# Optimization experiments

Hardware: AMD Instinct MI355X
Metric: run time of the kernel (lower is better)

The kernel has to match this reference:

```python
import jax, jax.numpy as jnp
from jax import lax
import numpy as np

N, T, C, H, W, S = 1, 8, 64, 192, 192, 4
HS, WS = H // S, W // S
CH = C * S * S          # 1024 = channels
G = 4                   # n_groups
CG = CH // G            # 256 = n_group_channels
ORF = 2.0               # offset_range_factor


def _unfold(x, s=S):
    # F.unfold(kernel=s, stride=s): (n,c,h,w) -> (n, c*s*s, (h//s)*(w//s))
    n, c, h, w = x.shape
    x = x.reshape(n, c, h // s, s, w // s, s).transpose(0, 1, 3, 5, 2, 4)
    return x.reshape(n, c * s * s, (h // s) * (w // s))


def _fold(x, h, w, s=S):
    # inverse of _unfold (non-overlapping)
    n, cl, _ = x.shape
    c = cl // (s * s)
    x = x.reshape(n, c, s, s, h // s, w // s).transpose(0, 1, 4, 2, 5, 3)
    return x.reshape(n, c, h, w)


def _gather_hw(x, iy, ix):
    # x (B,C,H,W); iy/ix (B,Hg,Wg) int32 -> (B,C,Hg,Wg)
    B, Cc, Hh, Ww = x.shape
    idx = (iy * Ww + ix).reshape(B, 1, -1)
    v = jnp.take_along_axis(x.reshape(B, Cc, Hh * Ww), idx, axis=2)
    return v.reshape(B, Cc, iy.shape[1], iy.shape[2])


def gs_nearest(x, grid):
    # F.grid_sample(mode='nearest', padding='zeros', align_corners=True)
    B, Cc, Hh, Ww = x.shape
    ix = (grid[..., 0] + 1.0) * 0.5 * (Ww - 1)
    iy = (grid[..., 1] + 1.0) * 0.5 * (Hh - 1)
    ixn = jnp.round(ix).astype(jnp.int32)
    iyn = jnp.round(iy).astype(jnp.int32)
    valid = (ixn >= 0) & (ixn < Ww) & (iyn >= 0) & (iyn < Hh)
    v = _gather_hw(x, jnp.clip(iyn, 0, Hh - 1), jnp.clip(ixn, 0, Ww - 1))
    return v * valid[:, None].astype(x.dtype)


def gs_bilinear(x, grid):
    # F.grid_sample(mode='bilinear', padding='zeros', align_corners=True)
    B, Cc, Hh, Ww = x.shape
    ix = (grid[..., 0] + 1.0) * 0.5 * (Ww - 1)
    iy = (grid[..., 1] + 1.0) * 0.5 * (Hh - 1)
    x0 = jnp.floor(ix)
    y0 = jnp.floor(iy)
    wx = ix - x0
    wy = iy - y0
    x0 = x0.astype(jnp.int32)
    y0 = y0.astype(jnp.int32)
    out = jnp.zeros((B, Cc) + grid.shape[1:3], x.dtype)
    for dy, dx in ((0, 0), (0, 1), (1, 0), (1, 1)):
        yi = y0 + dy
        xi = x0 + dx
        wgt = (wy if dy else 1.0 - wy) * (wx if dx else 1.0 - wx)
        valid = (xi >= 0) & (xi < Ww) & (yi >= 0) & (yi < Hh)
        v = _gather_hw(x, jnp.clip(yi, 0, Hh - 1), jnp.clip(xi, 0, Ww - 1))
        out = out + v * (wgt * valid)[:, None].astype(x.dtype)
    return out


def conv(x, w, b=None, pad=0, groups=1):
    y = lax.conv_general_dilated(x, w, (1, 1), [(pad, pad), (pad, pad)],
                                 dimension_numbers=('NCHW', 'OIHW', 'NCHW'),
                                 feature_group_count=groups)
    return y if b is None else y + b[None, :, None, None]


def ln_c(x, g, b, eps=1e-5):
    # LayerNormProxy: LayerNorm over channel dim of NCHW
    m = x.mean(axis=1, keepdims=True)
    v = ((x - m) ** 2).mean(axis=1, keepdims=True)
    return (x - m) / jnp.sqrt(v + eps) * g[None, :, None, None] + b[None, :, None, None]


def l2n(x, axis):
    return x / jnp.maximum(jnp.linalg.norm(x, axis=axis, keepdims=True), 1e-12)


def refpts(B, Hk, Wk, dt):
    ry = (jnp.linspace(0.5, Hk - 0.5, Hk, dtype=dt) / Hk) * 2 - 1
    rx = (jnp.linspace(0.5, Wk - 0.5, Wk, dtype=dt) / Wk) * 2 - 1
    ref = jnp.stack(jnp.meshgrid(ry, rx, indexing='ij'), axis=-1)  # (Hk,Wk,2)=(y,x)
    return jnp.broadcast_to(ref[None], (B, Hk, Wk, 2))


def _forward(cf, idx1, af, s1, s2, s3, loc, wtdw, btdw, lng, lnb, wtpw, wfus, bfus):
    n, c, h, w = af.shape
    t = s1.shape[1]
    hs, ws = h // S, w // S
    fl = c * S * S           # feat_len = 1024
    fn = hs * ws             # feat_num
    # trajectory locations -> normalized nearest-sampling grid
    gf = loc.reshape(n, t, 2, hs, ws).transpose(0, 1, 3, 4, 2)
    gx = 2.0 * gf[..., 0] / max(ws - 1, 1) - 1.0
    gy = 2.0 * gf[..., 1] / max(hs - 1, 1) - 1.0
    grid = jnp.stack((gx, gy), axis=-1).reshape(n * t, hs, ws, 2)
    o1 = gs_nearest(s1.reshape(n * t, fl, hs, ws), grid)
    o2 = gs_nearest(s2.reshape(n * t, fl, hs, ws), grid)
    o3 = gs_nearest(s3.reshape(n * t, fl, hs, ws), grid)
    oi = gs_nearest(idx1.reshape(n * t, fl, hs, ws), grid)
    oi = l2n(oi.reshape(n, t, fl, fn).transpose(0, 3, 1, 2), 3)   # (n,fn,t,fl)
    cu = _unfold(cf)                                              # (n,fl,fn)
    cn = l2n(cu.transpose(0, 2, 1), 2)                            # (n,fn,fl)
    tq = cn.reshape(n, hs, ws, fl).transpose(0, 3, 1, 2)          # (n,fl,hs,ws)
    tk = oi.transpose(0, 2, 1, 3).reshape(n * t, hs, ws, fl).transpose(0, 3, 1, 2)
    # deformable time offsets (grouped)
    qo = jnp.tile(tq.reshape(n * G, CG, hs, ws), (t, 1, 1, 1))
    ko = tk.reshape(n * t * G, CG, hs, ws)
    off = jnp.concatenate([qo, ko], axis=1)
    o = conv(off, wtdw, btdw, pad=2, groups=CG)
    o = ln_c(o, lng, lnb)
    o = jax.nn.gelu(o, approximate=False)
    o = conv(o, wtpw)                                             # (b,2,Hk,Wk)
    Hk, Wk = o.shape[2], o.shape[3]
    o = jnp.tanh(o) * jnp.array([1.0 / Hk, 1.0 / Wk], o.dtype).reshape(1, 2, 1, 1) * ORF
    pos = o.transpose(0, 2, 3, 1) + refpts(n * t * G, Hk, Wk, o.dtype)  # (b,Hk,Wk,(y,x))
    gp = pos[..., ::-1]                                           # (x,y) for grid_sample
    ks_ = gs_bilinear(tk.reshape(n * t * G, CG, hs, ws), gp)
    # '(n t g) c h w -> n (h w) t (g c)'
    ks_ = ks_.reshape(n, t, G, CG, Hk, Wk).transpose(0, 4, 5, 1, 2, 3).reshape(n, fn, t, fl)
    mat = jnp.einsum('nftc,nfc->nft', ks_, cn)
    csoft = mat.max(axis=2)
    cidx = mat.argmax(axis=2)
    csoft_f = _fold(jnp.broadcast_to(csoft[:, None, :], (n, fl, fn)), h, w)

    def sg(os_):
        v = gs_bilinear(os_.reshape(n * t * G, CG, hs, ws), gp).reshape(n, t, fl, fn)
        v = jnp.take_along_axis(v, cidx[:, None, None, :], axis=1)[:, 0]
        return _fold(v, h, w)

    out = conv(jnp.concatenate([sg(o1), sg(o2), sg(o3)], axis=1), wfus, bfus, pad=1)
    return out * csoft_f + af


def setup_inputs() -> dict:
    key = jax.random.key(0)
    ks = jax.random.split(key, 12)
    sc = 0.05
    return {
        'curr_feat': jax.random.normal(ks[0], (N, C, H, W), jnp.float32),
        'index_feat_set_s1': jax.random.normal(ks[1], (N, T, CH, HS, WS), jnp.float32),
        'anchor_feat': jax.random.normal(ks[2], (N, C, H, W), jnp.float32),
        'sparse_feat_set_s1': jax.random.normal(ks[3], (N, T, CH, HS, WS), jnp.float32),
        'sparse_feat_set_s2': jax.random.normal(ks[4], (N, T, CH, HS, WS), jnp.float32),
        'sparse_feat_set_s3': jax.random.normal(ks[5], (N, T, CH, HS, WS), jnp.float32),
        'location_feat': jax.random.uniform(ks[6], (N, 2 * T, HS, WS), jnp.float32) * (WS - 1.0),
        'w_tdw': jax.random.normal(ks[7], (CG, 2, 5, 5), jnp.float32) * sc,
        'b_tdw': jnp.zeros((CG,), jnp.float32),
        'ln_g': jnp.ones((CG,), jnp.float32),
        'ln_b': jnp.zeros((CG,), jnp.float32),
        'w_tpw': jax.random.normal(ks[8], (2, CG, 1, 1), jnp.float32) * sc,
        'w_fus': jax.random.normal(ks[9], (C, 3 * C, 3, 3), jnp.float32) * sc,
        'b_fus': jnp.zeros((C,), jnp.float32),
    }


def reference(curr_feat, index_feat_set_s1, anchor_feat, sparse_feat_set_s1, sparse_feat_set_s2, sparse_feat_set_s3, location_feat, w_tdw, b_tdw, ln_g, ln_b, w_tpw, w_fus, b_fus):
    return _forward(curr_feat, index_feat_set_s1, anchor_feat, sparse_feat_set_s1,
                    sparse_feat_set_s2, sparse_feat_set_s3, location_feat,
                    w_tdw, b_tdw, ln_g, ln_b, w_tpw, w_fus, b_fus)
```

## Files before the change

### kernel.cpp

```cpp
#include <hip/hip_runtime.h>
#include <math.h>

#define TT 8
#define FN 2304
#define FL 1024
#define HS 48

typedef __attribute__((ext_vector_type(8))) short short8;
typedef __attribute__((ext_vector_type(4))) float floatx4;

static constexpr size_t OFF_IDX1T  = 0;
static constexpr size_t OFF_SEL    = 75497472;
static constexpr size_t OFF_FIN    = 103809024;
static constexpr size_t OFF_WB     = 132713472;
static constexpr size_t OFF_NORM2  = 135497472;
static constexpr size_t OFF_PSRC   = 135571200;
static constexpr size_t OFF_PSCALE = 135644928;
static constexpr size_t OFF_CN     = 150994944;
static constexpr size_t OFF_QH     = 160432128;
static constexpr size_t OFF_SRCMAP = 165150720;
static constexpr size_t OFF_BSRC   = 165224448;
static constexpr size_t OFF_BW     = 166404096;
static constexpr size_t OFF_CSOFT  = 167583744;
static constexpr size_t OFF_CIDX   = 167592960;
static constexpr size_t OFF_CSRC   = 167602176;
static constexpr size_t OFF_CW     = 167749632;

__device__ inline ushort f2bf(float x) {
  union { float f; unsigned int u; } v; v.f = x;
  unsigned int r = (v.u + 0x7FFFu + ((v.u >> 16) & 1u)) >> 16;
  return (ushort)r;
}

__global__ void k_nearmap(const float* __restrict__ loc, int* __restrict__ srcmap,
                          float* __restrict__ norm2) {
  int idx = blockIdx.x * 256 + threadIdx.x;
  if (idx >= TT * FN) return;
  norm2[idx] = 0.f;
  int t = idx / FN, f = idx % FN;
  float lx = loc[(size_t)(t * 2 + 0) * FN + f];
  float ly = loc[(size_t)(t * 2 + 1) * FN + f];
  float gx = 2.0f * lx / 47.0f - 1.0f;
  float gy = 2.0f * ly / 47.0f - 1.0f;
  float ix = (gx + 1.0f) * 0.5f * 47.0f;
  float iy = (gy + 1.0f) * 0.5f * 47.0f;
  int ixn = __float2int_rn(ix);
  int iyn = __float2int_rn(iy);
  bool valid = (ixn >= 0) && (ixn < 48) && (iyn >= 0) && (iyn < 48);
  srcmap[idx] = valid ? (iyn * 48 + ixn) : -1;
}

__global__ __launch_bounds__(256) void k_transpose(const float* __restrict__ in, float* __restrict__ out,
                                                   float* __restrict__ norm2) {
  __shared__ float tile[64][65];
  const int t = blockIdx.z;
  const int cl0 = blockIdx.x * 64;
  const int f0 = blockIdx.y * 64;
  const float* src = in + (size_t)t * FL * FN;
  float* dst = out + (size_t)t * FN * FL;
  const int tx = threadIdx.x & 15, ty = threadIdx.x >> 4;
#pragma unroll
  for (int k = 0; k < 4; k++) {
    const float4 v = *reinterpret_cast<const float4*>(src + (size_t)(cl0 + ty + 16 * k) * FN + f0 + tx * 4);
    float* tr = &tile[ty + 16 * k][tx * 4];
    tr[0] = v.x; tr[1] = v.y; tr[2] = v.z; tr[3] = v.w;
  }
  __syncthreads();
#pragma unroll
  for (int k = 0; k < 4; k++) {
    float4 v;
    v.x = tile[tx * 4 + 0][ty + 16 * k];
    v.y = tile[tx * 4 + 1][ty + 16 * k];
    v.z = tile[tx * 4 + 2][ty + 16 * k];
    v.w = tile[tx * 4 + 3][ty + 16 * k];
    *reinterpret_cast<float4*>(dst + (size_t)(f0 + ty + 16 * k) * FL + cl0 + tx * 4) = v;
    float ss = v.x * v.x + v.y * v.y + v.z * v.z + v.w * v.w;
    ss += __shfl_xor(ss, 1, 64);
    ss += __shfl_xor(ss, 2, 64);
    ss += __shfl_xor(ss, 4, 64);
    ss += __shfl_xor(ss, 8, 64);
    if (tx == 0) atomicAdd(&norm2[(size_t)t * FN + f0 + ty + 16 * k], ss);
  }
}

__global__ void k_pos(const int* __restrict__ srcmap, const float* __restrict__ norm2,
                      int* __restrict__ psrc, float* __restrict__ pscale) {
  int idx = blockIdx.x * 256 + threadIdx.x;
  if (idx >= TT * FN) return;
  int s = srcmap[idx];
  int t = idx / FN;
  if (s < 0) {
    psrc[idx] = 0; pscale[idx] = 0.f;
  } else {
    psrc[idx] = s;
    float n2 = norm2[t * FN + s];
    pscale[idx] = 1.0f / fmaxf(sqrtf(n2), 1e-12f);
  }
}

__global__ __launch_bounds__(256) void k_cn(const float* __restrict__ cf, float* __restrict__ cn) {
  __shared__ float red[4];
  int f = blockIdx.x;
  int i = f / 48, j = f % 48;
  int tid = threadIdx.x;
  float v[4];
  float sq = 0.f;
#pragma unroll
  for (int k = 0; k < 4; k++) {
    int cl = tid + 256 * k;
    int c = cl >> 4, sy = (cl >> 2) & 3, sx = cl & 3;
    v[k] = cf[(size_t)c * 36864 + (size_t)(i * 4 + sy) * 192 + (j * 4 + sx)];
    sq += v[k] * v[k];
  }
#pragma unroll
  for (int m = 1; m <= 32; m <<= 1) sq += __shfl_xor(sq, m, 64);
  int lane = tid & 63, w = tid >> 6;
  if (lane == 0) red[w] = sq;
  __syncthreads();
  float total = red[0] + red[1] + red[2] + red[3];
  float scale = 1.0f / fmaxf(sqrtf(total), 1e-12f);
#pragma unroll
  for (int k = 0; k < 4; k++) cn[(size_t)f * FL + tid + 256 * k] = v[k] * scale;
}

__global__ __launch_bounds__(128) void k_qconv(const float* __restrict__ cn,
                                               const float* __restrict__ wtdw,
                                               const float* __restrict__ btdw,
                                               float* __restrict__ qhalf) {
  const int i = blockIdx.x;
  const int xcd = i & 7;
  const int sl = i >> 3;
  const int g = xcd >> 1;
  const int r0 = (xcd & 1) * 72 + sl;
  const int y = r0 / 3;
  const int xt = r0 - y * 3;
  const int j = threadIdx.x;
  const int x0 = xt * 16;
  float w0[25], w1[25];
  {
    const float* wp = wtdw + (size_t)j * 50;
#pragma unroll
    for (int p = 0; p < 25; ++p) { w0[p] = wp[p]; w1[p] = wp[25 + p]; }
  }
  float acc[16];
#pragma unroll
  for (int i2 = 0; i2 < 16; ++i2) acc[i2] = 0.f;
  const int cbase = g * 256 + 2 * j;
#pragma unroll
  for (int r = 0; r < 5; ++r) {
    const int yy = y - 2 + r;
    if (yy < 0 || yy >= 48) continue;
#pragma unroll
    for (int cc2 = 0; cc2 < 20; ++cc2) {
      const int xx = x0 - 2 + cc2;
      float vx = 0.f, vy = 0.f;
      if (xx >= 0 && xx < 48) {
        const float2 v = *reinterpret_cast<const float2*>(cn + ((size_t)(yy * 48 + xx) << 10) + cbase);
        vx = v.x; vy = v.y;
      }
#pragma unroll
      for (int kx = 0; kx < 5; ++kx) {
        const int xo = cc2 - kx;
        if (xo >= 0 && xo < 16)
          acc[xo] = fmaf(vx, w0[r * 5 + kx], fmaf(vy, w1[r * 5 + kx], acc[xo]));
      }
    }
  }
  const float bb = btdw[j];
#pragma unroll
  for (int xo = 0; xo < 16; ++xo)
    qhalf[((size_t)g * FN + (y * 48 + x0 + xo)) * 128 + j] = acc[xo] + bb;
}

__global__ __launch_bounds__(128) void k_kconv_ln(const float* __restrict__ idx1t,
                                                  const int* __restrict__ psrc,
                                                  const float* __restrict__ pscale,
                                                  const float* __restrict__ wtdw,
                                                  const float* __restrict__ btdw,
                                                  const float* __restrict__ qhalf,
                                                  const float* __restrict__ lng,
                                                  const float* __restrict__ lnb,
                                                  const float* __restrict__ wtpw,
                                                  int* __restrict__ bsrc,
                                                  float* __restrict__ bw) {
  __shared__ float ch[16][257];
  __shared__ int   s_ps[100];
  __shared__ float s_sc[100];
  const int ib = blockIdx.x;
  const int xcd = ib & 7;
  const int sl = ib >> 3;
  const int b = xcd + 8 * (sl / 144);
  const int r0 = sl % 144;
  const int y = r0 / 3;
  const int xt = r0 - y * 3;
  const int t = b >> 2, g = b & 3;
  const int j = threadIdx.x;
  const int x0 = xt * 16;
  const int tp = t * FN;

  if (j < 100) {
    const int rr = j / 20, cc = j - rr * 20;
    const int yy = y - 2 + rr, xx = x0 - 2 + cc;
    int sv = 0; float sc = 0.f;
    if ((unsigned)yy < 48u && (unsigned)xx < 48u) {
      const int p = tp + yy * 48 + xx;
      sv = psrc[p]; sc = pscale[p];
    }
    s_ps[j] = sv; s_sc[j] = sc;
  }

  float w0[25], w1[25];
  {
    const float* wp = wtdw + (size_t)(128 + j) * 50;
#pragma unroll
    for (int p = 0; p < 25; ++p) { w0[p] = wp[p]; w1[p] = wp[25 + p]; }
  }
  float acc[16];
#pragma unroll
  for (int i2 = 0; i2 < 16; ++i2) acc[i2] = 0.f;
  const int cbase = g * 256 + 2 * j;
  __syncthreads();
#pragma unroll
  for (int r = 0; r < 5; ++r) {
    const int yy = y - 2 + r;
    if (yy < 0 || yy >= 48) continue;
#pragma unroll
    for (int cc2 = 0; cc2 < 20; ++cc2) {
      const int s2 = s_ps[r * 20 + cc2];
      const float sc = s_sc[r * 20 + cc2];
      const float2 v = *reinterpret_cast<const float2*>(idx1t + (((size_t)tp + s2) << 10) + cbase);
      const float vx = v.x * sc, vy = v.y * sc;
#pragma unroll
      for (int kx = 0; kx < 5; ++kx) {
        const int xo = cc2 - kx;
        if (xo >= 0 && xo < 16)
          acc[xo] = fmaf(vx, w0[r * 5 + kx], fmaf(vy, w1[r * 5 + kx], acc[xo]));
      }
    }
  }
  const float bb = btdw[128 + j];
#pragma unroll
  for (int xo = 0; xo < 16; ++xo) ch[xo][128 + j] = acc[xo] + bb;
#pragma unroll
  for (int xo = 0; xo < 16; ++xo)
    ch[xo][j] = qhalf[((size_t)g * FN + (y * 48 + x0 + xo)) * 128 + j];
  __syncthreads();

  const int lane = j & 63, wv = j >> 6;
  for (int p = wv; p < 16; p += 2) {
    float v0 = ch[p][lane], v1 = ch[p][lane + 64], v2 = ch[p][lane + 128], v3 = ch[p][lane + 192];
    float s = v0 + v1 + v2 + v3;
    float q = v0 * v0 + v1 * v1 + v2 * v2 + v3 * v3;
#pragma unroll
    for (int m = 1; m <= 32; m <<= 1) { s += __shfl_xor(s, m, 64); q += __shfl_xor(q, m, 64); }
    float mean = s * (1.0f / 256.0f);
    float var = q * (1.0f / 256.0f) - mean * mean;
    float rstd = rsqrtf(var + 1e-5f);
    float d0 = 0.f, d1 = 0.f;
#pragma unroll
    for (int k2 = 0; k2 < 4; k2++) {
      int c = lane + 64 * k2;
      float xv = (k2 == 0) ? v0 : (k2 == 1) ? v1 : (k2 == 2) ? v2 : v3;
      float xn = (xv - mean) * rstd * lng[c] + lnb[c];
      float ge = 0.5f * xn * (1.0f + erff(xn * 0.70710678118654752440f));
      d0 += ge * wtpw[c];
      d1 += ge * wtpw[256 + c];
    }
#pragma unroll
    for (int m = 1; m <= 32; m <<= 1) { d0 += __shfl_xor(d0, m, 64); d1 += __shfl_xor(d1, m, 64); }
    if (lane == 0) {
      float o0 = tanhf(d0) * (2.0f / 48.0f);
      float o1 = tanhf(d1) * (2.0f / 48.0f);
      int x = x0 + p;
      float ry = (0.5f + (float)y) / 48.0f * 2.0f - 1.0f;
      float rx = (0.5f + (float)x) / 48.0f * 2.0f - 1.0f;
      float pos0 = o0 + ry, pos1 = o1 + rx;
      float ix = (pos1 + 1.0f) * 0.5f * 47.0f;
      float iy = (pos0 + 1.0f) * 0.5f * 47.0f;
      float x0f = floorf(ix), y0f = floorf(iy);
      float wx = ix - x0f, wy = iy - y0f;
      int xi = (int)x0f, yi = (int)y0f;
      size_t base = ((size_t)b * FN + y * 48 + x) * 4;
#pragma unroll
      for (int c = 0; c < 4; c++) {
        int dy = c >> 1, dx = c & 1;
        int yy2 = yi + dy, xx2 = xi + dx;
        bool ok = ((unsigned)yy2 < 48u) && ((unsigned)xx2 < 48u);
        float wgt = (dy ? wy : 1.0f - wy) * (dx ? wx : 1.0f - wx);
        bsrc[base + c] = ok ? (yy2 * 48 + xx2) : -1;
        bw[base + c] = wgt;
      }
    }
  }
}

__global__ __launch_bounds__(256) void k_mat(const float* __restrict__ idx1t,
                                             const int* __restrict__ psrc,
                                             const float* __restrict__ pscale,
                                             const float* __restrict__ cn,
                                             const int* __restrict__ bsrc,
                                             const float* __restrict__ bw,
                                             float* __restrict__ csoft,
                                             int* __restrict__ cidx) {
  __shared__ float red[8][4];
  const int f = blockIdx.x;
  const int tid = threadIdx.x;
  const int lane = tid & 63, w = tid >> 6;
  const int coff = w * 256 + lane * 4;
  const float4 cnv = *reinterpret_cast<const float4*>(cn + (size_t)f * FL + coff);
#pragma unroll
  for (int t = 0; t < TT; t++) {
    const size_t mb = ((size_t)(t * 4 + w) * FN + f) * 4;
    const int4 cs = *reinterpret_cast<const int4*>(bsrc + mb);
    const float4 wv = *reinterpret_cast<const float4*>(bw + mb);
    const int tp = t * FN;
    const float* base = idx1t + ((size_t)tp << 10) + coff;
    float ax = 0.f, ay = 0.f, az = 0.f, aw = 0.f;
    if (cs.x >= 0) { const float wsc = wv.x * pscale[tp + cs.x];
      const float4 u = *reinterpret_cast<const float4*>(base + ((size_t)psrc[tp + cs.x] << 10));
      ax = fmaf(wsc, u.x, ax); ay = fmaf(wsc, u.y, ay); az = fmaf(wsc, u.z, az); aw = fmaf(wsc, u.w, aw); }
    if (cs.y >= 0) { const float wsc = wv.y * pscale[tp + cs.y];
      const float4 u = *reinterpret_cast<const float4*>(base + ((size_t)psrc[tp + cs.y] << 10));
      ax = fmaf(wsc, u.x, ax); ay = fmaf(wsc, u.y, ay); az = fmaf(wsc, u.z, az); aw = fmaf(wsc, u.w, aw); }
    if (cs.z >= 0) { const float wsc = wv.z * pscale[tp + cs.z];
      const float4 u = *reinterpret_cast<const float4*>(base + ((size_t)psrc[tp + cs.z] << 10));
      ax = fmaf(wsc, u.x, ax); ay = fmaf(wsc, u.y, ay); az = fmaf(wsc, u.z, az); aw = fmaf(wsc, u.w, aw); }
    if (cs.w >= 0) { const float wsc = wv.w * pscale[tp + cs.w];
      const float4 u = *reinterpret_cast<const float4*>(base + ((size_t)psrc[tp + cs.w] << 10));
      ax = fmaf(wsc, u.x, ax); ay = fmaf(wsc, u.y, ay); az = fmaf(wsc, u.z, az); aw = fmaf(wsc, u.w, aw); }
    float partial = ax * cnv.x + ay * cnv.y + az * cnv.z + aw * cnv.w;
#pragma unroll
    for (int m = 1; m <= 32; m <<= 1) partial += __shfl_xor(partial, m, 64);
    if (lane == 0) red[t][w] = partial;
  }
  __syncthreads();
  if (tid == 0) {
    float bestv = -INFINITY;
    int besti = 0;
#pragma unroll
    for (int t = 0; t < TT; t++) {
      float tot = red[t][0] + red[t][1] + red[t][2] + red[t][3];
      if (tot > bestv) { bestv = tot; besti = t; }
    }
    csoft[f] = bestv; cidx[f] = besti;
  }
}

__global__ void k_comp(const int* __restrict__ bsrc, const float* __restrict__ bw,
                       const int* __restrict__ cidx, const int* __restrict__ srcmap,
                       int* __restrict__ csrc, float* __restrict__ cw) {
  int idx = blockIdx.x * 256 + threadIdx.x;
  if (idx >= FN * 4) return;
  int f = idx >> 2, g = idx & 3;
  int t = cidx[f];
  int b = t * 4 + g;
  size_t mb = ((size_t)b * FN + f) * 4;
  size_t ob = (size_t)idx * 4;
#pragma unroll
  for (int c = 0; c < 4; c++) {
    int s = bsrc[mb + c];
    csrc[ob + c] = (s >= 0) ? srcmap[t * FN + s] : -1;
    cw[ob + c] = bw[mb + c];
  }
}

__global__ __launch_bounds__(256) void k_sel(const float* __restrict__ s1,
                                             const float* __restrict__ s2,
                                             const float* __restrict__ s3,
                                             const int* __restrict__ cidx,
                                             const int* __restrict__ csrc,
                                             const float* __restrict__ cw,
                                             float* __restrict__ sel) {
  __shared__ float pl[4 * FN];
  const int cl = blockIdx.x, m = blockIdx.y;
  const float* sm = (m == 0) ? s1 : (m == 1) ? s2 : s3;
  const int g = cl >> 8;
  const int tid = threadIdx.x;
  float acc[9];
  int tsel[9];
  int4 cs[9];
  float4 wv[9];
#pragma unroll
  for (int it = 0; it < 9; it++) {
    int f = tid + 256 * it;
    tsel[it] = cidx[f];
    cs[it] = *reinterpret_cast<const int4*>(csrc + ((size_t)f * 4 + g) * 4);
    wv[it] = *reinterpret_cast<const float4*>(cw + ((size_t)f * 4 + g) * 4);
    acc[it] = 0.f;
  }
  float4* pl4 = reinterpret_cast<float4*>(pl);
  for (int half = 0; half < 2; half++) {
    __syncthreads();
#pragma unroll
    for (int j = 0; j < 9; j++) {
      const int e = j * 256 + tid;
      const int tl = e / 576;
      const int r = e - tl * 576;
      const float4* src4 = reinterpret_cast<const float4*>(sm + ((size_t)(half * 4 + tl) * FL + cl) * FN);
      pl4[e] = src4[r];
    }
    __syncthreads();
#pragma unroll
    for (int it = 0; it < 9; it++) {
      const int t = tsel[it] - half * 4;
      if (t >= 0 && t < 4) {
        float a = 0.f;
        if (cs[it].x >= 0) a += wv[it].x * pl[t * FN + cs[it].x];
        if (cs[it].y >= 0) a += wv[it].y * pl[t * FN + cs[it].y];
        if (cs[it].z >= 0) a += wv[it].z * pl[t * FN + cs[it].z];
        if (cs[it].w >= 0) a += wv[it].w * pl[t * FN + cs[it].w];
        acc[it] = a;
      }
    }
  }
  __syncthreads();
#pragma unroll
  for (int it = 0; it < 9; it++) pl[tid + 256 * it] = acc[it];
  __syncthreads();
  float4* orow = reinterpret_cast<float4*>(sel + ((size_t)m * FL + cl) * FN);
#pragma unroll
  for (int e = tid; e < 576; e += 256) orow[e] = pl4[e];
}

__global__ void k_zb(unsigned int* __restrict__ fin_u) {
  int idx = blockIdx.x * 256 + threadIdx.x;
  if (idx >= 772 * 96) return;
  int bp = idx / 96, u = idx % 96;
  int yy, xx;
  if (bp < 194)      { yy = 0;   xx = bp; }
  else if (bp < 388) { yy = 193; xx = bp - 194; }
  else if (bp < 580) { yy = bp - 388 + 1; xx = 0; }
  else               { yy = bp - 580 + 1; xx = 193; }
  fin_u[((size_t)yy * 194 + xx) * 96 + u] = 0;
}

__global__ __launch_bounds__(256) void k_fold2(const float* __restrict__ sel,
                                               ushort* __restrict__ fin) {
  __shared__ float ld[256 * 49];
  const int fy = blockIdx.x;
  const int m = blockIdx.y >> 2, c2t = blockIdx.y & 3;
  const int t = threadIdx.x;
  const float* sp = sel + ((size_t)m * 1024 + c2t * 256) * 2304 + fy * 48;
#pragma unroll
  for (int j = 0; j < 12; j++) {
    const int e = t + 256 * j;
    const int cl_l = e / 12, c4 = e % 12;
    const float4 v = *reinterpret_cast<const float4*>(sp + (size_t)cl_l * 2304 + c4 * 4);
    float* dr = &ld[cl_l * 49 + c4 * 4];
    dr[0] = v.x; dr[1] = v.y; dr[2] = v.z; dr[3] = v.w;
  }
  __syncthreads();
  const int ci0 = m * 64 + c2t * 16 + (t & 3) * 4;
  const int xb = t >> 2;
#pragma unroll
  for (int py = 0; py < 4; py++) {
    for (int jx = 0; jx < 3; jx++) {
      const int x = xb + 64 * jx;
      const int px = x & 3, fx = x >> 2;
      ushort4 v;
      ushort* vp = (ushort*)&v;
#pragma unroll
      for (int jj = 0; jj < 4; jj++) {
        int cl_l = ((t & 3) * 4 + jj) * 16 + py * 4 + px;
        vp[jj] = f2bf(ld[cl_l * 49 + fx]);
      }
      *reinterpret_cast<ushort4*>(fin + (((size_t)(fy * 4 + py + 1) * 194) + x + 1) * 192 + ci0) = v;
    }
  }
}

__global__ void k_wb(const float* __restrict__ wfus, ushort* __restrict__ wb) {
  int idx = blockIdx.x * 256 + threadIdx.x;
  if (idx >= 64 * 9 * 96) return;
  int cp = idx % 96, tap = (idx / 96) % 9, co = idx / (96 * 9);
  int ci = cp * 2;
  float a = wfus[((size_t)co * 192 + ci) * 9 + tap];
  float b = wfus[((size_t)co * 192 + ci + 1) * 9 + tap];
  unsigned int pk = (unsigned int)f2bf(a) | ((unsigned int)f2bf(b) << 16);
  reinterpret_cast<unsigned int*>(wb)[((size_t)co * 9 + tap) * 96 + cp] = pk;
}

__global__ __launch_bounds__(256) void k_fus(const ushort* __restrict__ fin,
                                             const ushort* __restrict__ wb,
                                             const float* __restrict__ bfus,
                                             const float* __restrict__ csoft,
                                             const float* __restrict__ af,
                                             float* __restrict__ out) {
  const int y = blockIdx.x;
  const int wv = threadIdx.x >> 6;
  const int l = threadIdx.x & 63;
  const int ln = l & 15, qd = l >> 4;
  const int x0 = wv * 48;
  floatx4 acc[4][3];
#pragma unroll
  for (int a = 0; a < 4; a++)
#pragma unroll
    for (int b = 0; b < 3; b++) acc[a][b] = (floatx4){0.f, 0.f, 0.f, 0.f};

  const int koff = qd * 8;
  for (int tap = 0; tap < 9; tap++) {
    const int ky = tap / 3, kx = tap % 3;
    const ushort* brow = fin + ((size_t)(y + ky) * 194 + kx) * 192;
    const ushort* wrow = wb + (size_t)tap * 192;
#pragma unroll
    for (int c6 = 0; c6 < 6; c6++) {
      const int ci = c6 * 32 + koff;
      short8 A[4], B[3];
#pragma unroll
      for (int mt = 0; mt < 4; mt++)
        A[mt] = *reinterpret_cast<const short8*>(wrow + (size_t)(mt * 16 + ln) * 1728 + ci);
#pragma unroll
      for (int nt = 0; nt < 3; nt++)
        B[nt] = *reinterpret_cast<const short8*>(brow + (size_t)(x0 + nt * 16 + ln) * 192 + ci);
#pragma unroll
      for (int mt = 0; mt < 4; mt++)
#pragma unroll
        for (int nt = 0; nt < 3; nt++)
          acc[mt][nt] = __builtin_amdgcn_mfma_f32_16x16x32_bf16(A[mt], B[nt], acc[mt][nt], 0, 0, 0);
    }
  }
#pragma unroll
  for (int nt = 0; nt < 3; nt++) {
    const int x = x0 + nt * 16 + ln;
    const float cs = csoft[(y >> 2) * 48 + (x >> 2)];
#pragma unroll
    for (int mt = 0; mt < 4; mt++) {
#pragma unroll
      for (int r = 0; r < 4; r++) {
        const int co = mt * 16 + qd * 4 + r;
        const size_t oi = (size_t)co * 36864 + (size_t)y * 192 + x;
        out[oi] = (acc[mt][nt][r] + bfus[co]) * cs + af[oi];
      }
    }
  }
}

extern "C" void kernel_launch(void* const* d_in, const int* in_sizes, int n_in,
                              void* d_out, int out_size, void* d_ws, size_t ws_size,
                              hipStream_t stream) {
  const float* cf   = (const float*)d_in[0];
  const float* idx1 = (const float*)d_in[1];
  const float* af   = (const float*)d_in[2];
  const float* s1   = (const float*)d_in[3];
  const float* s2   = (const float*)d_in[4];
  const float* s3   = (const float*)d_in[5];
  const float* loc  = (const float*)d_in[6];
  const float* wtdw = (const float*)d_in[7];
  const float* btdw = (const float*)d_in[8];
  const float* lng  = (const float*)d_in[9];
  const float* lnb  = (const float*)d_in[10];
  const float* wtpw = (const float*)d_in[11];
  const float* wfus = (const float*)d_in[12];
  const float* bfus = (const float*)d_in[13];
  float* out = (float*)d_out;
  char* ws = (char*)d_ws;

  float* idx1t  = (float*)(ws + OFF_IDX1T);
  float* sel    = (float*)(ws + OFF_SEL);
  ushort* fin   = (ushort*)(ws + OFF_FIN);
  ushort* wb    = (ushort*)(ws + OFF_WB);
  float* norm2  = (float*)(ws + OFF_NORM2);
  int*   psrc   = (int*)(ws + OFF_PSRC);
  float* pscale = (float*)(ws + OFF_PSCALE);
  float* cn     = (float*)(ws + OFF_CN);
  float* qh     = (float*)(ws + OFF_QH);
  int*   srcmap = (int*)(ws + OFF_SRCMAP);
  int*   bsrc   = (int*)(ws + OFF_BSRC);
  float* bw     = (float*)(ws + OFF_BW);
  float* csoft  = (float*)(ws + OFF_CSOFT);
  int*   cidx   = (int*)(ws + OFF_CIDX);
  int*   csrc   = (int*)(ws + OFF_CSRC);
  float* cw     = (float*)(ws + OFF_CW);

  k_nearmap<<<72, 256, 0, stream>>>(loc, srcmap, norm2);
  k_transpose<<<dim3(16, 36, 8), 256, 0, stream>>>(idx1, idx1t, norm2);
  k_cn<<<2304, 256, 0, stream>>>(cf, cn);
  k_pos<<<72, 256, 0, stream>>>(srcmap, norm2, psrc, pscale);
  k_wb<<<216, 256, 0, stream>>>(wfus, wb);
  k_zb<<<290, 256, 0, stream>>>((unsigned int*)fin);
  k_qconv<<<576, 128, 0, stream>>>(cn, wtdw, btdw, qh);
  k_kconv_ln<<<4608, 128, 0, stream>>>(idx1t, psrc, pscale, wtdw, btdw, qh, lng, lnb, wtpw, bsrc, bw);
  k_mat<<<2304, 256, 0, stream>>>(idx1t, psrc, pscale, cn, bsrc, bw, csoft, cidx);
  k_comp<<<36, 256, 0, stream>>>(bsrc, bw, cidx, srcmap, csrc, cw);
  k_sel<<<dim3(1024, 3), 256, 0, stream>>>(s1, s2, s3, cidx, csrc, cw, sel);
  k_fold2<<<dim3(48, 12), 256, 0, stream>>>(sel, fin);
  k_fus<<<192, 256, 0, stream>>>(fin, wb, bfus, csoft, af, out);
}
```

Measured before the change: 525.0 us.

## Double-buffer k_sel plane loads via direct global-to-LDS with packed registers

Rewrites the k_sel gather so each of the 8 time planes is streamed into a double-buffered 2xFN shared array using global_load_lds. The load of plane s+1 overlaps with computing plane s. Per-thread source indices and time selectors are bit-packed into 32-bit words and the bilinear weights are stored as half2, cutting register use. Launch bounds now target 6 blocks per CU, which together with the smaller LDS footprint is meant to raise occupancy. The trade-off is lower precision on the weights (fp16) and more barriers, one per plane instead of per half.

```diff
diff --git a/kernel.cpp b/kernel.cpp
--- a/kernel.cpp
+++ b/kernel.cpp
@@ -1,4 +1,5 @@
 #include <hip/hip_runtime.h>
+#include <hip/hip_fp16.h>
 #include <math.h>
 
 #define TT 8
@@ -30,6 +31,12 @@
   union { float f; unsigned int u; } v; v.f = x;
   unsigned int r = (v.u + 0x7FFFu + ((v.u >> 16) & 1u)) >> 16;
   return (ushort)r;
+}
+
+__device__ __forceinline__ void gload_lds16(const float* g, float* l) {
+  __builtin_amdgcn_global_load_lds(
+      (const __attribute__((address_space(1))) unsigned int*)(g),
+      (__attribute__((address_space(3))) unsigned int*)(l), 16, 0, 0);
 }
 
 __global__ void k_nearmap(const float* __restrict__ loc, int* __restrict__ srcmap,
@@ -364,61 +371,79 @@
   }
 }
 
-__global__ __launch_bounds__(256) void k_sel(const float* __restrict__ s1,
-                                             const float* __restrict__ s2,
-                                             const float* __restrict__ s3,
-                                             const int* __restrict__ cidx,
-                                             const int* __restrict__ csrc,
-                                             const float* __restrict__ cw,
-                                             float* __restrict__ sel) {
-  __shared__ float pl[4 * FN];
+__global__ __launch_bounds__(256, 6) void k_sel(const float* __restrict__ s1,
+                                                const float* __restrict__ s2,
+                                                const float* __restrict__ s3,
+                                                const int* __restrict__ cidx,
+                                                const int* __restrict__ csrc,
+                                                const float* __restrict__ cw,
+                                                float* __restrict__ sel) {
+  __shared__ float buf[2][FN];
   const int cl = blockIdx.x, m = blockIdx.y;
   const float* sm = (m == 0) ? s1 : (m == 1) ? s2 : s3;
   const int g = cl >> 8;
   const int tid = threadIdx.x;
+  const int lane = tid & 63, wid = tid >> 6;
+
+  unsigned int pk0[9], pk1[9], wh01[9], wh23[9];
   float acc[9];
-  int tsel[9];
-  int4 cs[9];
-  float4 wv[9];
 #pragma unroll
   for (int it = 0; it < 9; it++) {
-    int f = tid + 256 * it;
-    tsel[it] = cidx[f];
-    cs[it] = *reinterpret_cast<const int4*>(csrc + ((size_t)f * 4 + g) * 4);
-    wv[it] = *reinterpret_cast<const float4*>(cw + ((size_t)f * 4 + g) * 4);
+    const int f = tid + 256 * it;
+    const unsigned int ts = (unsigned int)cidx[f];
+    const int4 cs = *reinterpret_cast<const int4*>(csrc + ((size_t)f * 4 + g) * 4);
+    const float4 wv = *reinterpret_cast<const float4*>(cw + ((size_t)f * 4 + g) * 4);
+    const unsigned int c0 = (cs.x >= 0) ? (unsigned int)cs.x : 0x1FFFu;
+    const unsigned int c1 = (cs.y >= 0) ? (unsigned int)cs.y : 0x1FFFu;
+    const unsigned int c2 = (cs.z >= 0) ? (unsigned int)cs.z : 0x1FFFu;
+    const unsigned int c3 = (cs.w >= 0) ? (unsigned int)cs.w : 0x1FFFu;
+    pk0[it] = c0 | (c1 << 13) | (ts << 26);
+    pk1[it] = c2 | (c3 << 13);
+    __half2 h01 = __floats2half2_rn(wv.x, wv.y);
+    __half2 h23 = __floats2half2_rn(wv.z, wv.w);
+    wh01[it] = *reinterpret_cast<unsigned int*>(&h01);
+    wh23[it] = *reinterpret_cast<unsigned int*>(&h23);
     acc[it] = 0.f;
   }
-  float4* pl4 = reinterpret_cast<float4*>(pl);
-  for (int half = 0; half < 2; half++) {
-    __syncthreads();
-#pragma unroll
-    for (int j = 0; j < 9; j++) {
-      const int e = j * 256 + tid;
-      const int tl = e / 576;
-      const int r = e - tl * 576;
-      const float4* src4 = reinterpret_cast<const float4*>(sm + ((size_t)(half * 4 + tl) * FL + cl) * FN);
-      pl4[e] = src4[r];
-    }
-    __syncthreads();
+
+  {
+    const float* pb = sm + (size_t)cl * FN;
+    for (int c = wid; c < 9; c += 4)
+      gload_lds16(pb + c * 256 + lane * 4, &buf[0][c * 256]);
+  }
+  __syncthreads();
+
+  for (int s = 0; s < TT; s++) {
+    if (s + 1 < TT) {
+      const float* pb = sm + ((size_t)(s + 1) * FL + cl) * FN;
+      float* lb = &buf[(s + 1) & 1][0];
+      for (int c = wid; c < 9; c += 4)
+        gload_lds16(pb + c * 256 + lane * 4, lb + c * 256);
+    }
+    const float* lb = &buf[s & 1][0];
 #pragma unroll
     for (int it = 0; it < 9; it++) {
-      const int t = tsel[it] - half * 4;
-      if (t >= 0 && t < 4) {
+      if ((int)(pk0[it] >> 26) == s) {
+        const unsigned int a0 = pk0[it] & 0x1FFFu, a1 = (pk0[it] >> 13) & 0x1FFFu;
+        const unsigned int a2 = pk1[it] & 0x1FFFu, a3 = (pk1[it] >> 13) & 0x1FFFu;
+        const float2 w01 = __half22float2(*reinterpret_cast<const __half2*>(&wh01[it]));
+        const float2 w23 = __half22float2(*reinterpret_cast<const __half2*>(&wh23[it]));
         float a = 0.f;
-        if (cs[it].x >= 0) a += wv[it].x * pl[t * FN + cs[it].x];
-        if (cs[it].y >= 0) a += wv[it].y * pl[t * FN + cs[it].y];
-        if (cs[it].z >= 0) a += wv[it].z * pl[t * FN + cs[it].z];
-        if (cs[it].w >= 0) a += wv[it].w * pl[t * FN + cs[it].w];
+        if (a0 < FN) a = fmaf(w01.x, lb[a0], a);
+        if (a1 < FN) a = fmaf(w01.y, lb[a1], a);
+        if (a2 < FN) a = fmaf(w23.x, lb[a2], a);
+        if (a3 < FN) a = fmaf(w23.y, lb[a3], a);
         acc[it] = a;
       }
     }
-  }
-  __syncthreads();
-#pragma unroll
-  for (int it = 0; it < 9; it++) pl[tid + 256 * it] = acc[it];
-  __syncthreads();
+    __syncthreads();
+  }
+
+#pragma unroll
+  for (int it = 0; it < 9; it++) buf[0][tid + 256 * it] = acc[it];
+  __syncthreads();
+  const float4* pl4 = reinterpret_cast<const float4*>(&buf[0][0]);
   float4* orow = reinterpret_cast<float4*>(sel + ((size_t)m * FL + cl) * FN);
-#pragma unroll
   for (int e = tid; e < 576; e += 256) orow[e] = pl4[e];
 }
 
```

After: 683.6 us. 1.3x slower.

## Bucket positions by selected frame so k_sel loads only needed time planes

Applied to the files above, without the earlier changes.

A new single-block kernel buckets the spatial positions by their selected time index, producing a compact position list and offsets per frame. k_sel now launches one block per (frame, channel, source) and returns early for frames nobody selected. Each block loads just that frame's plane into LDS via global_load_lds DMA instead of streaming all eight planes. The block ordering is remapped across XCDs. This is meant to cut redundant global reads of unused frames. The cost is many more, smaller blocks, scattered output writes, and an extra launch. Bucket buffers reuse the bsrc workspace region after k_comp has consumed it.

```diff
diff --git a/kernel.cpp b/kernel.cpp
--- a/kernel.cpp
+++ b/kernel.cpp
@@ -1,4 +1,5 @@
 #include <hip/hip_runtime.h>
+#include <hip/hip_fp16.h>
 #include <math.h>
 
 #define TT 8
@@ -20,6 +21,8 @@
 static constexpr size_t OFF_QH     = 160432128;
 static constexpr size_t OFF_SRCMAP = 165150720;
 static constexpr size_t OFF_BSRC   = 165224448;
+static constexpr size_t OFF_FLIST  = OFF_BSRC;
+static constexpr size_t OFF_FOFF   = OFF_BSRC + 9216;
 static constexpr size_t OFF_BW     = 166404096;
 static constexpr size_t OFF_CSOFT  = 167583744;
 static constexpr size_t OFF_CIDX   = 167592960;
@@ -30,6 +33,12 @@
   union { float f; unsigned int u; } v; v.f = x;
   unsigned int r = (v.u + 0x7FFFu + ((v.u >> 16) & 1u)) >> 16;
   return (ushort)r;
+}
+
+__device__ __forceinline__ void gload_lds16(const float* g, float* l) {
+  __builtin_amdgcn_global_load_lds(
+      (const __attribute__((address_space(1))) unsigned int*)(g),
+      (__attribute__((address_space(3))) unsigned int*)(l), 16, 0, 0);
 }
 
 __global__ void k_nearmap(const float* __restrict__ loc, int* __restrict__ srcmap,
@@ -364,62 +373,69 @@
   }
 }
 
+__global__ void k_bucket(const int* __restrict__ cidx, int* __restrict__ flist,
+                         int* __restrict__ foff) {
+  __shared__ int cnt[8];
+  __shared__ int base[8];
+  const int tid = threadIdx.x;
+  if (tid < 8) cnt[tid] = 0;
+  __syncthreads();
+  for (int f = tid; f < FN; f += 256) atomicAdd(&cnt[cidx[f]], 1);
+  __syncthreads();
+  if (tid == 0) {
+    int s = 0;
+    for (int t = 0; t < 8; t++) { base[t] = s; foff[t] = s; s += cnt[t]; }
+    foff[8] = s;
+  }
+  __syncthreads();
+  for (int f = tid; f < FN; f += 256) {
+    int t = cidx[f];
+    int p = atomicAdd(&base[t], 1);
+    flist[p] = f;
+  }
+}
+
 __global__ __launch_bounds__(256) void k_sel(const float* __restrict__ s1,
                                              const float* __restrict__ s2,
                                              const float* __restrict__ s3,
-                                             const int* __restrict__ cidx,
+                                             const int* __restrict__ flist,
+                                             const int* __restrict__ foff,
                                              const int* __restrict__ csrc,
                                              const float* __restrict__ cw,
                                              float* __restrict__ sel) {
-  __shared__ float pl[4 * FN];
-  const int cl = blockIdx.x, m = blockIdx.y;
+  __shared__ float pl[FN];
+  const int i = blockIdx.x;
+  const int xcd = i & 7;
+  const int b = i >> 3;
+  const int t = b & 7;
+  const int job = xcd * 384 + (b >> 3);
+  const int m = job >> 10;
+  const int cl = job & 1023;
+  const int tid = threadIdx.x;
+  const int lane = tid & 63, wid = tid >> 6;
+
+  const int o0 = foff[t], o1 = foff[t + 1];
+  if (o0 == o1) return;
+
   const float* sm = (m == 0) ? s1 : (m == 1) ? s2 : s3;
+  const float* pb = sm + ((size_t)t * FL + cl) * FN;
+  for (int c = wid; c < 9; c += 4)
+    gload_lds16(pb + c * 256 + lane * 4, &pl[c * 256]);
+  __syncthreads();
+
   const int g = cl >> 8;
-  const int tid = threadIdx.x;
-  float acc[9];
-  int tsel[9];
-  int4 cs[9];
-  float4 wv[9];
-#pragma unroll
-  for (int it = 0; it < 9; it++) {
-    int f = tid + 256 * it;
-    tsel[it] = cidx[f];
-    cs[it] = *reinterpret_cast<const int4*>(csrc + ((size_t)f * 4 + g) * 4);
-    wv[it] = *reinterpret_cast<const float4*>(cw + ((size_t)f * 4 + g) * 4);
-    acc[it] = 0.f;
-  }
-  float4* pl4 = reinterpret_cast<float4*>(pl);
-  for (int half = 0; half < 2; half++) {
-    __syncthreads();
-#pragma unroll
-    for (int j = 0; j < 9; j++) {
-      const int e = j * 256 + tid;
-      const int tl = e / 576;
-      const int r = e - tl * 576;
-      const float4* src4 = reinterpret_cast<const float4*>(sm + ((size_t)(half * 4 + tl) * FL + cl) * FN);
-      pl4[e] = src4[r];
-    }
-    __syncthreads();
-#pragma unroll
-    for (int it = 0; it < 9; it++) {
-      const int t = tsel[it] - half * 4;
-      if (t >= 0 && t < 4) {
-        float a = 0.f;
-        if (cs[it].x >= 0) a += wv[it].x * pl[t * FN + cs[it].x];
-        if (cs[it].y >= 0) a += wv[it].y * pl[t * FN + cs[it].y];
-        if (cs[it].z >= 0) a += wv[it].z * pl[t * FN + cs[it].z];
-        if (cs[it].w >= 0) a += wv[it].w * pl[t * FN + cs[it].w];
-        acc[it] = a;
-      }
-    }
-  }
-  __syncthreads();
-#pragma unroll
-  for (int it = 0; it < 9; it++) pl[tid + 256 * it] = acc[it];
-  __syncthreads();
-  float4* orow = reinterpret_cast<float4*>(sel + ((size_t)m * FL + cl) * FN);
-#pragma unroll
-  for (int e = tid; e < 576; e += 256) orow[e] = pl4[e];
+  float* orow = sel + ((size_t)m * FL + cl) * FN;
+  for (int ii = o0 + tid; ii < o1; ii += 256) {
+    const int f = flist[ii];
+    const int4 cs = *reinterpret_cast<const int4*>(csrc + ((size_t)f * 4 + g) * 4);
+    const float4 wv = *reinterpret_cast<const float4*>(cw + ((size_t)f * 4 + g) * 4);
+    float a = 0.f;
+    if (cs.x >= 0) a = fmaf(wv.x, pl[cs.x], a);
+    if (cs.y >= 0) a = fmaf(wv.y, pl[cs.y], a);
+    if (cs.z >= 0) a = fmaf(wv.z, pl[cs.z], a);
+    if (cs.w >= 0) a = fmaf(wv.w, pl[cs.w], a);
+    orow[f] = a;
+  }
 }
 
 __global__ void k_zb(unsigned int* __restrict__ fin_u) {
@@ -566,6 +582,8 @@
   float* qh     = (float*)(ws + OFF_QH);
   int*   srcmap = (int*)(ws + OFF_SRCMAP);
   int*   bsrc   = (int*)(ws + OFF_BSRC);
+  int*   flist  = (int*)(ws + OFF_FLIST);
+  int*   foff   = (int*)(ws + OFF_FOFF);
   float* bw     = (float*)(ws + OFF_BW);
   float* csoft  = (float*)(ws + OFF_CSOFT);
   int*   cidx   = (int*)(ws + OFF_CIDX);
@@ -582,7 +600,8 @@
   k_kconv_ln<<<4608, 128, 0, stream>>>(idx1t, psrc, pscale, wtdw, btdw, qh, lng, lnb, wtpw, bsrc, bw);
   k_mat<<<2304, 256, 0, stream>>>(idx1t, psrc, pscale, cn, bsrc, bw, csoft, cidx);
   k_comp<<<36, 256, 0, stream>>>(bsrc, bw, cidx, srcmap, csrc, cw);
-  k_sel<<<dim3(1024, 3), 256, 0, stream>>>(s1, s2, s3, cidx, csrc, cw, sel);
+  k_bucket<<<1, 256, 0, stream>>>(cidx, flist, foff);
+  k_sel<<<24576, 256, 0, stream>>>(s1, s2, s3, flist, foff, csrc, cw, sel);
   k_fold2<<<dim3(48, 12), 256, 0, stream>>>(sel, fin);
   k_fus<<<192, 256, 0, stream>>>(fin, wb, bfus, csoft, af, out);
 }
```

Measured after the change: 591.7 us. 12.7% more time.
